# Performance work log

Measured on AMD Instinct MI355X. Metric: run time of the kernel, lower is better.

Reference implementation:

```python
import jax, jax.numpy as jnp
import numpy as np

STACK = 1000            # stackSize (number of stacked TT networks, e.g. relations)
L = (8, 8, 8)           # input_fac[0]: left mode sizes  -> nRow = 512
R = (8, 8, 8)           # input_fac[1]: right mode sizes -> nCol = 512
RANKS = (16, 16)        # internal TT ranks (boundary ranks of 1 are dropped)
B = 512                 # batch of indices


def setup_inputs() -> dict:
    key = jax.random.key(0)
    k0, k1, k2, ki = jax.random.split(key, 4)
    # torch.rand(coreSize) * 0.1  ->  uniform[0, 0.1)
    core0 = jax.random.uniform(k0, (STACK, L[0], R[0], RANKS[0]), dtype=jnp.float32) * 0.1
    core1 = jax.random.uniform(k1, (STACK, RANKS[0], L[1], R[1], RANKS[1]), dtype=jnp.float32) * 0.1
    core2 = jax.random.uniform(k2, (STACK, RANKS[1], L[2], R[2]), dtype=jnp.float32) * 0.1
    indices = jax.random.randint(ki, (B,), 0, STACK, dtype=jnp.int64 if jax.config.read('jax_enable_x64') else jnp.int32)
    return {"core0": core0, "core1": core1, "core2": core2, "indices": indices}


def reference(core0, core1, core2, indices):
    # Gather the per-index TT cores
    c0 = core0[indices]  # [b, l0, r0, k1]
    c1 = core1[indices]  # [b, k1, l1, r1, k2]
    c2 = core2[indices]  # [b, k2, l2, r2]
    # Sequential TT-chain contraction over rank axes k1 then k2.
    # ncon out_order = [batch, l0, l1, l2, r0, r1, r2]
    t = jnp.einsum('baik,bkcjm->bacijm', c0, c1)        # [b, l0, l1, r0, r1, k2]
    out = jnp.einsum('bacijm,bmdl->bacdijl', t, c2)     # [b, l0, l1, l2, r0, r1, r2]
    nRow = L[0] * L[1] * L[2]
    nCol = R[0] * R[1] * R[2]
    return out.reshape(indices.shape[0], nRow, nCol)
```

## Files before the change

### kernel.cpp

```cpp
#include <hip/hip_runtime.h>
#include <stdint.h>


typedef short short8 __attribute__((ext_vector_type(8)));
typedef float f32x4 __attribute__((ext_vector_type(4)));

__device__ __forceinline__ uint32_t pack_bf2(float f0, float f1) {
  uint32_t a = __float_as_uint(f0) + 0x8000u;
  uint32_t b = __float_as_uint(f1) + 0x8000u;
  return (a >> 16) | (b & 0xffff0000u);
}

__global__ __launch_bounds__(256, 4) void tt_stack_kernel(
    const float* __restrict__ c0f,
    const float* __restrict__ c1f,
    const float* __restrict__ c2f,
    const int* __restrict__ idx,
    float* __restrict__ outf)
{
  __shared__ __align__(16) uint32_t lds_t[4096];

  const int tid = threadIdx.x;
  const int bid = blockIdx.x;
  const int b = bid & 511;
  const int a = bid >> 9;
  const int s = idx[b];
  const size_t s1024 = (size_t)s * 1024;

  const int lane = tid & 63, wv = tid >> 6;
  const int g = lane >> 4, lcol = lane & 15;

  short8 Afr[4];
  {
    const float* c2s = c2f + s1024 + (size_t)((g & 1) * 8) * 64;
#pragma unroll
    for (int rt = 0; rt < 4; ++rt) {
      const int col = rt * 16 + lcol;
      uint32_t w[4];
#pragma unroll
      for (int p = 0; p < 4; ++p) {
        const float v0 = c2s[(2 * p) * 64 + col];
        const float v1 = c2s[(2 * p + 1) * 64 + col];
        const uint32_t h0 = (__float_as_uint(v0) + 0x8000u) & 0xffff0000u;
        const uint32_t h1 = (__float_as_uint(v1) + 0x8000u) & 0xffff0000u;
        const uint32_t hip = (h0 >> 16) | h1;
        const uint32_t lop = pack_bf2(v0 - __uint_as_float(h0),
                                      v1 - __uint_as_float(h1));
        w[p] = (g < 2) ? hip : lop;
      }
      uint4 wq = make_uint4(w[0], w[1], w[2], w[3]);
      Afr[rt] = *reinterpret_cast<short8*>(&wq);
    }
  }

  const int i = (lane >> 3) & 7, j = lane & 7;
  float c0v[16];
  {
    const float* c0s = c0f + (size_t)(s * 8 + a) * 128 + i * 16;
#pragma unroll
    for (int q = 0; q < 4; ++q)
      *(f32x4*)&c0v[q * 4] = *(const f32x4*)(c0s + q * 4);
  }

  const int sw = (lane >> 2) & 1;
  const int hsel = (g & 1) ^ ((lcol >> 2) & 1);
  float* const outa = outf + (size_t)b * 262144 + a * 32768;

#pragma unroll
  for (int cc = 0; cc < 2; ++cc) {
    const int row = wv * 128 + cc * 64 + lane;
    const int c = wv * 2 + cc;
    const float* c1r = c1f + (size_t)s * 16384 + (size_t)(c * 8 + j) * 16;
    float acc[16];
#pragma unroll
    for (int m = 0; m < 16; ++m) acc[m] = 0.f;
#pragma unroll 2
    for (int k = 0; k < 16; ++k) {
      const f32x4* rp = (const f32x4*)(c1r + (size_t)k * 1024);
      const f32x4 v0 = rp[0];
      const f32x4 v1 = rp[1];
      const f32x4 v2 = rp[2];
      const f32x4 v3 = rp[3];
      const float av = c0v[k];
      acc[0]  = fmaf(av, v0[0], acc[0]);   acc[1]  = fmaf(av, v0[1], acc[1]);
      acc[2]  = fmaf(av, v0[2], acc[2]);   acc[3]  = fmaf(av, v0[3], acc[3]);
      acc[4]  = fmaf(av, v1[0], acc[4]);   acc[5]  = fmaf(av, v1[1], acc[5]);
      acc[6]  = fmaf(av, v1[2], acc[6]);   acc[7]  = fmaf(av, v1[3], acc[7]);
      acc[8]  = fmaf(av, v2[0], acc[8]);   acc[9]  = fmaf(av, v2[1], acc[9]);
      acc[10] = fmaf(av, v2[2], acc[10]);  acc[11] = fmaf(av, v2[3], acc[11]);
      acc[12] = fmaf(av, v3[0], acc[12]);  acc[13] = fmaf(av, v3[1], acc[13]);
      acc[14] = fmaf(av, v3[2], acc[14]);  acc[15] = fmaf(av, v3[3], acc[15]);
    }
    uint32_t* tb = &lds_t[row * 8];
    *(uint4*)&tb[sw * 4] =
        make_uint4(pack_bf2(acc[0], acc[1]),  pack_bf2(acc[2], acc[3]),
                   pack_bf2(acc[4], acc[5]),  pack_bf2(acc[6], acc[7]));
    *(uint4*)&tb[4 - sw * 4] =
        make_uint4(pack_bf2(acc[8], acc[9]),  pack_bf2(acc[10], acc[11]),
                   pack_bf2(acc[12], acc[13]), pack_bf2(acc[14], acc[15]));
  }

#pragma unroll
  for (int ctl = 0; ctl < 8; ++ctl) {
    const int cix = wv * 128 + ctl * 16 + lcol;
    const short8 bv8 = *(const short8*)&lds_t[cix * 8 + hsel * 4];
    const int cq = cix >> 6;
    const int klo = cix & 63;
    float* const op0 = outa + (size_t)(cq * 8 + (g >> 1)) * 512
                            + klo * 8 + (g & 1) * 4;
#pragma unroll
    for (int rt = 0; rt < 4; ++rt) {
      f32x4 dd = {0.f, 0.f, 0.f, 0.f};
      dd = __builtin_amdgcn_mfma_f32_16x16x32_bf16(Afr[rt], bv8, dd, 0, 0, 0);
      __builtin_nontemporal_store(dd, (f32x4*)(op0 + rt * 1024));
    }
  }
}

extern "C" void kernel_launch(void* const* d_in, const int* in_sizes, int n_in,
                              void* d_out, int out_size, void* d_ws, size_t ws_size,
                              hipStream_t stream) {
  const float* c0f = (const float*)d_in[0];
  const float* c1f = (const float*)d_in[1];
  const float* c2f = (const float*)d_in[2];
  const int* idx = (const int*)d_in[3];
  float* outf = (float*)d_out;
  const int B = in_sizes[3];
  dim3 grid(B * 8), block(256);
  hipLaunchKernelGGL(tt_stack_kernel, grid, block, 0, stream, c0f, c1f, c2f, idx, outf);
}
```

Before: 615.5 us.

## Stage core1 slice in LDS as bf16 and interleave per-wave chain stages

Each block now cooperatively loads its core1 slice (64KB fp32) into shared memory as packed bf16 before the first contraction, instead of each wave reading it from global memory per k. Block ordering is switched so the 8 blocks of one batch element are adjacent, which improves L2 reuse of the gathered cores. Each wave now contracts and immediately does its MFMA stage per half using a per-wave buffer. The change adds 32KB more LDS (reducing occupancy) and an extra bf16 rounding of core1, which adds precision error.

```diff
diff --git a/kernel.cpp b/kernel.cpp
--- a/kernel.cpp
+++ b/kernel.cpp
@@ -5,6 +5,8 @@
 typedef short short8 __attribute__((ext_vector_type(8)));
 typedef float f32x4 __attribute__((ext_vector_type(4)));
 
+__device__ __forceinline__ float bflo(uint32_t u) { return __uint_as_float(u << 16); }
+__device__ __forceinline__ float bfhi(uint32_t u) { return __uint_as_float(u & 0xffff0000u); }
 __device__ __forceinline__ uint32_t pack_bf2(float f0, float f1) {
   uint32_t a = __float_as_uint(f0) + 0x8000u;
   uint32_t b = __float_as_uint(f1) + 0x8000u;
@@ -18,17 +20,28 @@
     const int* __restrict__ idx,
     float* __restrict__ outf)
 {
-  __shared__ __align__(16) uint32_t lds_t[4096];
+  __shared__ __align__(16) uint32_t lds_c1[8192];
+  __shared__ __align__(16) uint32_t lds_t[2048];
 
   const int tid = threadIdx.x;
   const int bid = blockIdx.x;
-  const int b = bid & 511;
-  const int a = bid >> 9;
+  const int b = bid >> 3;
+  const int a = bid & 7;
   const int s = idx[b];
   const size_t s1024 = (size_t)s * 1024;
 
   const int lane = tid & 63, wv = tid >> 6;
   const int g = lane >> 4, lcol = lane & 15;
+
+  {
+    const float4* src4 = (const float4*)(c1f + (size_t)s * 16384);
+#pragma unroll
+    for (int r = 0; r < 16; ++r) {
+      const float4 v = src4[r * 256 + tid];
+      uint2* dst = (uint2*)&lds_c1[2 * (r * 256 + tid)];
+      *dst = make_uint2(pack_bf2(v.x, v.y), pack_bf2(v.z, v.w));
+    }
+  }
 
   short8 Afr[4];
   {
@@ -61,58 +74,53 @@
     for (int q = 0; q < 4; ++q)
       *(f32x4*)&c0v[q * 4] = *(const f32x4*)(c0s + q * 4);
   }
+  __syncthreads();
 
   const int sw = (lane >> 2) & 1;
   const int hsel = (g & 1) ^ ((lcol >> 2) & 1);
+  uint32_t* const tbuf = &lds_t[wv * 512];
   float* const outa = outf + (size_t)b * 262144 + a * 32768;
 
 #pragma unroll
-  for (int cc = 0; cc < 2; ++cc) {
-    const int row = wv * 128 + cc * 64 + lane;
-    const int c = wv * 2 + cc;
-    const float* c1r = c1f + (size_t)s * 16384 + (size_t)(c * 8 + j) * 16;
+  for (int h = 0; h < 2; ++h) {
+    const int c = wv * 2 + h;
     float acc[16];
 #pragma unroll
     for (int m = 0; m < 16; ++m) acc[m] = 0.f;
-#pragma unroll 2
+#pragma unroll
     for (int k = 0; k < 16; ++k) {
-      const f32x4* rp = (const f32x4*)(c1r + (size_t)k * 1024);
-      const f32x4 v0 = rp[0];
-      const f32x4 v1 = rp[1];
-      const f32x4 v2 = rp[2];
-      const f32x4 v3 = rp[3];
+      const uint4* rp = (const uint4*)&lds_c1[((k * 8 + c) * 8 + j) * 8];
+      const uint4 u0 = rp[0];
+      const uint4 u1 = rp[1];
       const float av = c0v[k];
-      acc[0]  = fmaf(av, v0[0], acc[0]);   acc[1]  = fmaf(av, v0[1], acc[1]);
-      acc[2]  = fmaf(av, v0[2], acc[2]);   acc[3]  = fmaf(av, v0[3], acc[3]);
-      acc[4]  = fmaf(av, v1[0], acc[4]);   acc[5]  = fmaf(av, v1[1], acc[5]);
-      acc[6]  = fmaf(av, v1[2], acc[6]);   acc[7]  = fmaf(av, v1[3], acc[7]);
-      acc[8]  = fmaf(av, v2[0], acc[8]);   acc[9]  = fmaf(av, v2[1], acc[9]);
-      acc[10] = fmaf(av, v2[2], acc[10]);  acc[11] = fmaf(av, v2[3], acc[11]);
-      acc[12] = fmaf(av, v3[0], acc[12]);  acc[13] = fmaf(av, v3[1], acc[13]);
-      acc[14] = fmaf(av, v3[2], acc[14]);  acc[15] = fmaf(av, v3[3], acc[15]);
+      acc[0]  = fmaf(av, bflo(u0.x), acc[0]);   acc[1]  = fmaf(av, bfhi(u0.x), acc[1]);
+      acc[2]  = fmaf(av, bflo(u0.y), acc[2]);   acc[3]  = fmaf(av, bfhi(u0.y), acc[3]);
+      acc[4]  = fmaf(av, bflo(u0.z), acc[4]);   acc[5]  = fmaf(av, bfhi(u0.z), acc[5]);
+      acc[6]  = fmaf(av, bflo(u0.w), acc[6]);   acc[7]  = fmaf(av, bfhi(u0.w), acc[7]);
+      acc[8]  = fmaf(av, bflo(u1.x), acc[8]);   acc[9]  = fmaf(av, bfhi(u1.x), acc[9]);
+      acc[10] = fmaf(av, bflo(u1.y), acc[10]);  acc[11] = fmaf(av, bfhi(u1.y), acc[11]);
+      acc[12] = fmaf(av, bflo(u1.z), acc[12]);  acc[13] = fmaf(av, bfhi(u1.z), acc[13]);
+      acc[14] = fmaf(av, bflo(u1.w), acc[14]);  acc[15] = fmaf(av, bfhi(u1.w), acc[15]);
     }
-    uint32_t* tb = &lds_t[row * 8];
-    *(uint4*)&tb[sw * 4] =
+    *(uint4*)&tbuf[lane * 8 + sw * 4] =
         make_uint4(pack_bf2(acc[0], acc[1]),  pack_bf2(acc[2], acc[3]),
                    pack_bf2(acc[4], acc[5]),  pack_bf2(acc[6], acc[7]));
-    *(uint4*)&tb[4 - sw * 4] =
+    *(uint4*)&tbuf[lane * 8 + 4 - sw * 4] =
         make_uint4(pack_bf2(acc[8], acc[9]),  pack_bf2(acc[10], acc[11]),
                    pack_bf2(acc[12], acc[13]), pack_bf2(acc[14], acc[15]));
-  }
 
 #pragma unroll
-  for (int ctl = 0; ctl < 8; ++ctl) {
-    const int cix = wv * 128 + ctl * 16 + lcol;
-    const short8 bv8 = *(const short8*)&lds_t[cix * 8 + hsel * 4];
-    const int cq = cix >> 6;
-    const int klo = cix & 63;
-    float* const op0 = outa + (size_t)(cq * 8 + (g >> 1)) * 512
-                            + klo * 8 + (g & 1) * 4;
+    for (int ctl = 0; ctl < 4; ++ctl) {
+      const int r = ctl * 16 + lcol;
+      const short8 bv8 = *(const short8*)&tbuf[r * 8 + hsel * 4];
+      float* const op0 = outa + (size_t)(c * 8 + (g >> 1)) * 512
+                              + r * 8 + (g & 1) * 4;
 #pragma unroll
-    for (int rt = 0; rt < 4; ++rt) {
-      f32x4 dd = {0.f, 0.f, 0.f, 0.f};
-      dd = __builtin_amdgcn_mfma_f32_16x16x32_bf16(Afr[rt], bv8, dd, 0, 0, 0);
-      __builtin_nontemporal_store(dd, (f32x4*)(op0 + rt * 1024));
+      for (int rt = 0; rt < 4; ++rt) {
+        f32x4 dd = {0.f, 0.f, 0.f, 0.f};
+        dd = __builtin_amdgcn_mfma_f32_16x16x32_bf16(Afr[rt], bv8, dd, 0, 0, 0);
+        __builtin_nontemporal_store(dd, (f32x4*)(op0 + rt * 1024));
+      }
     }
   }
 }
```

Result: faster. 574.1 us (-6.7%).
